# Optimization experiments

Hardware: AMD Instinct MI355X
Metric: run time of the kernel (lower is better)

## Reference

```python
import jax, jax.numpy as jnp
import numpy as np
from jax import lax

EXP = 5      # exponent bits of the custom float format
MAN = 10     # mantissa bits
STRIDE = 1
PADDING = 1


def float_quantize(x, exp=EXP, man=MAN):
    """Round-to-nearest-even quantization to a custom (exp, man) float format,
    with exponent clamping to the subnormal range and saturation at max value.
    Uses a straight-through estimator so the op is differentiable."""
    emax = 2 ** (exp - 1) - 1
    emin = 1 - emax
    _, e = jnp.frexp(x)                      # x = m * 2^e, m in [0.5, 1)
    e = jnp.maximum(e - 1, emin)             # unbiased exponent, clamp to emin (subnormals)
    scale = jnp.exp2((e - man).astype(x.dtype))
    q = jnp.round(x / scale) * scale         # round half to even on the mantissa grid
    maxval = jnp.asarray((2.0 - 2.0 ** (-man)) * 2.0 ** emax, x.dtype)
    q = jnp.clip(q, -maxval, maxval)
    return x + lax.stop_gradient(q - x)      # straight-through


def quant_gemm(a, b):
    """a: [M, K], b: [K, N]. FMA-style GEMM where the product and the running
    accumulator are re-quantized to the (EXP, MAN) format at every k step,
    mimicking the custom low-precision accumulation loop."""
    M = a.shape[0]
    N = b.shape[1]

    def step(acc, ab):
        ak, bk = ab                          # ak: [M], bk: [N]
        prod = float_quantize(ak[:, None] * bk[None, :])
        return float_quantize(acc + prod), None

    acc0 = jnp.zeros((M, N), a.dtype)
    acc, _ = lax.scan(step, acc0, (a.T, b))
    return acc


def _unfold(x, kh, kw, stride, padding):
    """im2col matching torch.nn.functional.unfold: returns [B, OH*OW, C*kh*kw]."""
    B, C, H, W = x.shape
    oh = (H - kh + 2 * padding) // stride + 1
    ow = (W - kw + 2 * padding) // stride + 1
    xp = jnp.pad(x, ((0, 0), (0, 0), (padding, padding), (padding, padding)))
    cols = []
    for i in range(kh):
        for j in range(kw):
            cols.append(xp[:, :, i:i + (oh - 1) * stride + 1:stride,
                              j:j + (ow - 1) * stride + 1:stride])
    col = jnp.stack(cols, axis=2)            # [B, C, kh*kw, oh, ow]
    col = col.reshape(B, C * kh * kw, oh * ow)
    return col.transpose(0, 2, 1), oh, ow    # [B, M, K]


def setup_inputs() -> dict:
    key = jax.random.key(0)
    kx, kw_, kb = jax.random.split(key, 3)
    x = jax.random.normal(kx, (16, 32, 56, 56), dtype=jnp.float32)
    # kaiming-uniform-ish scale: fan_in = 32*3*3 = 288
    weight = jax.random.normal(kw_, (64, 32, 3, 3), dtype=jnp.float32) * (1.0 / np.sqrt(288.0))
    bias = jax.random.normal(kb, (64,), dtype=jnp.float32) * (1.0 / np.sqrt(288.0))
    return {"x": x, "weight": weight, "bias": bias}


def reference(x, weight, bias):
    B, C, H, W = x.shape
    N, Cg, kh, kw = weight.shape
    qw = float_quantize(weight)              # quantize weights
    qb = float_quantize(bias)                # quantize bias
    a, oh, ow = _unfold(x, kh, kw, STRIDE, PADDING)   # [B, M, K]
    K = C * kh * kw
    a2 = a.reshape(B * oh * ow, K)
    b2 = qw.reshape(N, K).T                  # [K, N]
    out = quant_gemm(a2, b2)                 # [B*M, N], low-precision accumulation
    out = out + qb[None, :]
    out = float_quantize(out)                # re-quantize output
    out = out.reshape(B, oh * ow, N).transpose(0, 2, 1)
    return out.reshape(B, N, oh, ow)
```

## Files before the change

kernel.cpp:

```cpp
#include <hip/hip_runtime.h>
#include <stdint.h>

typedef _Float16 f16x8 __attribute__((ext_vector_type(8)));
typedef float    f32x4 __attribute__((ext_vector_type(4)));

#define H 56
#define W 56
#define C_IN 32
#define N_OUT 64
#define PR 58
#define PC 68
#define NPD (16 * C_IN * PR * 34)
#define LCS 124
#define NWF 9216

__device__ __forceinline__ float q16f(float v) { return (float)(_Float16)v; }

__global__ void prep_x(const float* __restrict__ x, uint32_t* __restrict__ xp) {
    int idx = blockIdx.x * 256 + threadIdx.x;
    if (idx >= NPD) return;
    int d   = idx % 34;
    int t   = idx / 34;
    int row = t % PR;
    int bc  = t / PR;
    int ih  = row - 1;
    int iw0 = 2 * d - 2, iw1 = 2 * d - 1;
    _Float16 lo = (_Float16)0.f, hi = (_Float16)0.f;
    if ((unsigned)ih < (unsigned)H) {
        const float* src = x + (size_t)(bc * H + ih) * W;
        if ((unsigned)iw0 < (unsigned)W) lo = (_Float16)src[iw0];
        if ((unsigned)iw1 < (unsigned)W) hi = (_Float16)src[iw1];
    }
    xp[idx] = (uint32_t)__builtin_bit_cast(uint16_t, lo) |
              ((uint32_t)__builtin_bit_cast(uint16_t, hi) << 16);
}

__global__ void prep_w(const float* __restrict__ weight, uint32_t* __restrict__ wf) {
    int o = blockIdx.x * 256 + threadIdx.x;
    if (o >= NWF) return;
    int j2   = o & 3;
    int lane = (o >> 2) & 63;
    int u    = o >> 8;
    int nt   = u & 3;
    int ij   = u >> 2;
    int n    = nt * 16 + (lane & 15);
    int c0   = (lane >> 4) * 8 + 2 * j2;
    _Float16 lo = (_Float16)weight[n * 288 + c0 * 9 + ij];
    _Float16 hi = (_Float16)weight[n * 288 + (c0 + 1) * 9 + ij];
    wf[o] = (uint32_t)__builtin_bit_cast(uint16_t, lo) |
            ((uint32_t)__builtin_bit_cast(uint16_t, hi) << 16);
}

__global__ __launch_bounds__(256, 4) void conv_mfma(
    const uint32_t* __restrict__ xp,
    const f16x8*    __restrict__ wf,
    const float*    __restrict__ bias,
    float* __restrict__ out)
{
    __shared__ uint32_t sX[C_IN * (LCS / 2)];

    const int tid = threadIdx.x;
    const int b   = blockIdx.z;
    const int oh0 = blockIdx.y * 4;
    const int ow0 = blockIdx.x * 16;

    {
        const int base_src = ((b * C_IN) * PR + oh0) * 34 + (ow0 >> 1);
        for (int i = tid; i < C_IN * 60; i += 256) {
            int c = i / 60, rem = i - c * 60;
            int r = rem / 10, d = rem - r * 10;
            sX[c * 62 + r * 10 + d] = xp[base_src + (c * PR + r) * 34 + d];
        }
    }
    __syncthreads();

    const int wid  = tid >> 6;
    const int lane = tid & 63;
    const int quad = lane >> 4;
    const int m    = lane & 15;
    const int oh   = oh0 + wid;

    const _Float16* sxh = (const _Float16*)sX;
    const int abase = quad * (8 * LCS) + wid * 20 + m + 1;

    f32x4 acc[4] = {{0,0,0,0},{0,0,0,0},{0,0,0,0},{0,0,0,0}};

    #pragma unroll
    for (int ij = 0; ij < 9; ++ij) {
        const int i  = ij / 3, jj = ij - 3 * i;
        const int sh = i * 20 + jj;

        f16x8 bfr[4];
        #pragma unroll
        for (int nt = 0; nt < 4; ++nt)
            bfr[nt] = wf[(ij * 4 + nt) * 64 + lane];

        f16x8 af;
        #pragma unroll
        for (int t = 0; t < 8; ++t)
            af[t] = sxh[abase + sh + t * LCS];

        #pragma unroll
        for (int nt = 0; nt < 4; ++nt)
            acc[nt] = __builtin_amdgcn_mfma_f32_16x16x32_f16(af, bfr[nt], acc[nt], 0, 0, 0);
    }

    const int ncol = lane & 15;
    #pragma unroll
    for (int nt = 0; nt < 4; ++nt) {
        const int n  = nt * 16 + ncol;
        const float qb = q16f(bias[n]);
        float* ob = out + ((size_t)(b * N_OUT + n) * H + oh) * W;
        #pragma unroll
        for (int reg = 0; reg < 4; ++reg) {
            const int ow = ow0 + quad * 4 + reg;
            if (ow < W) ob[ow] = q16f(acc[nt][reg] + qb);
        }
    }
}

extern "C" void kernel_launch(void* const* d_in, const int* in_sizes, int n_in,
                              void* d_out, int out_size, void* d_ws, size_t ws_size,
                              hipStream_t stream) {
    const float* x      = (const float*)d_in[0];
    const float* weight = (const float*)d_in[1];
    const float* bias   = (const float*)d_in[2];
    float* out          = (float*)d_out;

    uint32_t* xp = (uint32_t*)d_ws;
    uint32_t* wfp = (uint32_t*)((char*)d_ws + (size_t)NPD * 4);

    prep_x<<<dim3((NPD + 255) / 256), dim3(256), 0, stream>>>(x, xp);
    prep_w<<<dim3((NWF + 255) / 256), dim3(256), 0, stream>>>(weight, wfp);
    conv_mfma<<<dim3(4, 14, 16), dim3(256), 0, stream>>>(xp, (const f16x8*)wfp, bias, out);
}
```

Before: 85.71 us.

## Use channel-last fp16 padded input, fuse prep kernels, drop LDS staging in conv

The prep step now transposes x into an NHWC-style padded fp16 buffer through a shared-memory tile, and weight packing is folded into the same launch. The conv kernel loads each 8-channel MFMA fragment with one 16-byte global load instead of staging a tile in LDS and gathering eight scalar halves. It also swaps the MFMA operand roles so each lane holds one output pixel and writes are coalesced along width. This removes a kernel launch, the LDS copy, the barrier and strided scalar loads. In exchange the conv relies on L1/L2 for the overlapping 3x3 window reuse, and the transpose adds shared-memory work to prep.

```diff
diff --git a/kernel.cpp b/kernel.cpp
--- a/kernel.cpp
+++ b/kernel.cpp
@@ -9,112 +9,92 @@
 #define C_IN 32
 #define N_OUT 64
 #define PR 58
-#define PC 68
-#define NPD (16 * C_IN * PR * 34)
-#define LCS 124
+#define PCOLS 66
+#define XB_BLOCKS (16 * PR)
 #define NWF 9216
+#define XPAD_BYTES ((size_t)16 * PR * PCOLS * C_IN * 2)
 
 __device__ __forceinline__ float q16f(float v) { return (float)(_Float16)v; }
 
-__global__ void prep_x(const float* __restrict__ x, uint32_t* __restrict__ xp) {
-    int idx = blockIdx.x * 256 + threadIdx.x;
-    if (idx >= NPD) return;
-    int d   = idx % 34;
-    int t   = idx / 34;
-    int row = t % PR;
-    int bc  = t / PR;
-    int ih  = row - 1;
-    int iw0 = 2 * d - 2, iw1 = 2 * d - 1;
-    _Float16 lo = (_Float16)0.f, hi = (_Float16)0.f;
-    if ((unsigned)ih < (unsigned)H) {
-        const float* src = x + (size_t)(bc * H + ih) * W;
-        if ((unsigned)iw0 < (unsigned)W) lo = (_Float16)src[iw0];
-        if ((unsigned)iw1 < (unsigned)W) hi = (_Float16)src[iw1];
+__global__ __launch_bounds__(256) void prep_kernel(
+    const float* __restrict__ x, const float* __restrict__ weight,
+    _Float16* __restrict__ xpad, uint32_t* __restrict__ wf)
+{
+    const int nb  = blockIdx.x;
+    const int tid = threadIdx.x;
+    if (nb < XB_BLOCKS) {
+        __shared__ _Float16 sT[PCOLS * 34];
+        for (int i = tid; i < PCOLS * 17; i += 256) ((uint32_t*)sT)[i] = 0u;
+        __syncthreads();
+        const int b = nb / PR, row = nb % PR, ih = row - 1;
+        if ((unsigned)ih < (unsigned)H) {
+            #pragma unroll
+            for (int k = 0; k < 7; ++k) {
+                int idx = k * 256 + tid;
+                int c = idx / W, iw = idx - c * W;
+                sT[(iw + 1) * 34 + c] = (_Float16)x[((b * C_IN + c) * H + ih) * W + iw];
+            }
+        }
+        __syncthreads();
+        uint32_t* dst = (uint32_t*)(xpad + ((size_t)b * PR + row) * PCOLS * C_IN);
+        for (int i = tid; i < PCOLS * 16; i += 256) {
+            int col = i >> 4, cd = i & 15;
+            dst[i] = ((const uint32_t*)sT)[col * 17 + cd];
+        }
+    } else {
+        int o = (nb - XB_BLOCKS) * 256 + tid;
+        int t2   = o & 3;
+        int lane = (o >> 2) & 63;
+        int u    = o >> 8;
+        int nt   = u & 3, ij = u >> 2;
+        int n    = nt * 16 + (lane & 15);
+        int c0   = (lane >> 4) * 8 + 2 * t2;
+        _Float16 lo = (_Float16)weight[n * 288 + c0 * 9 + ij];
+        _Float16 hi = (_Float16)weight[n * 288 + (c0 + 1) * 9 + ij];
+        wf[o] = (uint32_t)__builtin_bit_cast(uint16_t, lo) |
+                ((uint32_t)__builtin_bit_cast(uint16_t, hi) << 16);
     }
-    xp[idx] = (uint32_t)__builtin_bit_cast(uint16_t, lo) |
-              ((uint32_t)__builtin_bit_cast(uint16_t, hi) << 16);
-}
-
-__global__ void prep_w(const float* __restrict__ weight, uint32_t* __restrict__ wf) {
-    int o = blockIdx.x * 256 + threadIdx.x;
-    if (o >= NWF) return;
-    int j2   = o & 3;
-    int lane = (o >> 2) & 63;
-    int u    = o >> 8;
-    int nt   = u & 3;
-    int ij   = u >> 2;
-    int n    = nt * 16 + (lane & 15);
-    int c0   = (lane >> 4) * 8 + 2 * j2;
-    _Float16 lo = (_Float16)weight[n * 288 + c0 * 9 + ij];
-    _Float16 hi = (_Float16)weight[n * 288 + (c0 + 1) * 9 + ij];
-    wf[o] = (uint32_t)__builtin_bit_cast(uint16_t, lo) |
-            ((uint32_t)__builtin_bit_cast(uint16_t, hi) << 16);
 }
 
 __global__ __launch_bounds__(256, 4) void conv_mfma(
-    const uint32_t* __restrict__ xp,
+    const _Float16* __restrict__ xpad,
     const f16x8*    __restrict__ wf,
     const float*    __restrict__ bias,
     float* __restrict__ out)
 {
-    __shared__ uint32_t sX[C_IN * (LCS / 2)];
-
-    const int tid = threadIdx.x;
-    const int b   = blockIdx.z;
-    const int oh0 = blockIdx.y * 4;
-    const int ow0 = blockIdx.x * 16;
-
-    {
-        const int base_src = ((b * C_IN) * PR + oh0) * 34 + (ow0 >> 1);
-        for (int i = tid; i < C_IN * 60; i += 256) {
-            int c = i / 60, rem = i - c * 60;
-            int r = rem / 10, d = rem - r * 10;
-            sX[c * 62 + r * 10 + d] = xp[base_src + (c * PR + r) * 34 + d];
-        }
-    }
-    __syncthreads();
-
-    const int wid  = tid >> 6;
+    const int tid  = threadIdx.x;
+    const int b    = blockIdx.z;
+    const int oh   = blockIdx.y * 4 + (tid >> 6);
+    const int ow0  = blockIdx.x * 16;
     const int lane = tid & 63;
     const int quad = lane >> 4;
-    const int m    = lane & 15;
-    const int oh   = oh0 + wid;
+    const int px   = lane & 15;
 
-    const _Float16* sxh = (const _Float16*)sX;
-    const int abase = quad * (8 * LCS) + wid * 20 + m + 1;
+    const _Float16* xb = xpad + (((size_t)b * PR + oh) * PCOLS + ow0 + px) * C_IN + quad * 8;
 
     f32x4 acc[4] = {{0,0,0,0},{0,0,0,0},{0,0,0,0},{0,0,0,0}};
 
     #pragma unroll
     for (int ij = 0; ij < 9; ++ij) {
-        const int i  = ij / 3, jj = ij - 3 * i;
-        const int sh = i * 20 + jj;
-
-        f16x8 bfr[4];
+        const int i = ij / 3, jj = ij - 3 * i;
+        f16x8 xf = *(const f16x8*)(xb + (i * PCOLS + jj) * C_IN);
         #pragma unroll
-        for (int nt = 0; nt < 4; ++nt)
-            bfr[nt] = wf[(ij * 4 + nt) * 64 + lane];
-
-        f16x8 af;
-        #pragma unroll
-        for (int t = 0; t < 8; ++t)
-            af[t] = sxh[abase + sh + t * LCS];
-
-        #pragma unroll
-        for (int nt = 0; nt < 4; ++nt)
-            acc[nt] = __builtin_amdgcn_mfma_f32_16x16x32_f16(af, bfr[nt], acc[nt], 0, 0, 0);
+        for (int nt = 0; nt < 4; ++nt) {
+            f16x8 wv = wf[(ij * 4 + nt) * 64 + lane];
+            acc[nt] = __builtin_amdgcn_mfma_f32_16x16x32_f16(wv, xf, acc[nt], 0, 0, 0);
+        }
     }
 
-    const int ncol = lane & 15;
-    #pragma unroll
-    for (int nt = 0; nt < 4; ++nt) {
-        const int n  = nt * 16 + ncol;
-        const float qb = q16f(bias[n]);
-        float* ob = out + ((size_t)(b * N_OUT + n) * H + oh) * W;
+    const int ow = ow0 + px;
+    if (ow < W) {
         #pragma unroll
-        for (int reg = 0; reg < 4; ++reg) {
-            const int ow = ow0 + quad * 4 + reg;
-            if (ow < W) ob[ow] = q16f(acc[nt][reg] + qb);
+        for (int nt = 0; nt < 4; ++nt) {
+            #pragma unroll
+            for (int reg = 0; reg < 4; ++reg) {
+                const int n = nt * 16 + quad * 4 + reg;
+                out[((size_t)(b * N_OUT + n) * H + oh) * W + ow] =
+                    q16f(acc[nt][reg] + q16f(bias[n]));
+            }
         }
     }
 }
@@ -127,10 +107,9 @@
     const float* bias   = (const float*)d_in[2];
     float* out          = (float*)d_out;
 
-    uint32_t* xp = (uint32_t*)d_ws;
-    uint32_t* wfp = (uint32_t*)((char*)d_ws + (size_t)NPD * 4);
+    _Float16* xpad = (_Float16*)d_ws;
+    uint32_t* wfp  = (uint32_t*)((char*)d_ws + XPAD_BYTES);
 
-    prep_x<<<dim3((NPD + 255) / 256), dim3(256), 0, stream>>>(x, xp);
-    prep_w<<<dim3((NWF + 255) / 256), dim3(256), 0, stream>>>(weight, wfp);
-    conv_mfma<<<dim3(4, 14, 16), dim3(256), 0, stream>>>(xp, (const f16x8*)wfp, bias, out);
+    prep_kernel<<<dim3(XB_BLOCKS + NWF / 256), dim3(256), 0, stream>>>(x, weight, xpad, wfp);
+    conv_mfma<<<dim3(4, 14, 16), dim3(256), 0, stream>>>(xpad, (const f16x8*)wfp, bias, out);
 }
```

Result: faster. 73.62 us (-14.1%).
